# Kernel tuning notes

Hardware: AMD Instinct MI355X
Metric: run time of the kernel (lower is better)

The kernel has to match this reference:

```python
import jax, jax.numpy as jnp
import numpy as np

NUM_MODELS = 64
IN_F, HID, OUT_F = 6, 64, 3
LAYERS = 5
LN_EPS = 1e-5


def _mm_linear(x, W, B, idx):
    # W: [M, out, in], B: [M, out], x: [N, in], idx: [N]
    return jnp.einsum('nof,nf->no', W[idx], x) + B[idx]


def _mm_layernorm(x, g, b, idx):
    mu = jnp.mean(x, axis=-1, keepdims=True)
    var = jnp.mean((x - mu) ** 2, axis=-1, keepdims=True)
    xn = (x - mu) * jax.lax.rsqrt(var + LN_EPS)
    return xn * g[idx] + b[idx]


def setup_inputs() -> dict:
    key = jax.random.key(0)
    ks = jax.random.split(key, 16)
    N = 262144
    sqrt_k = float(np.sqrt(1.0 / NUM_MODELS))
    u = lambda k, shape: jax.random.uniform(k, shape, jnp.float32, -sqrt_k, sqrt_k)
    inp = {
        'x': jax.random.normal(ks[0], (N, IN_F), jnp.float32),
        'indices': jax.random.randint(ks[1], (N,), 0, NUM_MODELS),
        'W0': u(ks[2], (NUM_MODELS, HID, IN_F)), 'B0': u(ks[3], (NUM_MODELS, HID)),
        'G0': jnp.ones((NUM_MODELS, HID), jnp.float32), 'H0': jnp.zeros((NUM_MODELS, HID), jnp.float32),
        'W1': u(ks[4], (NUM_MODELS, HID, HID)), 'B1': u(ks[5], (NUM_MODELS, HID)),
        'G1': jnp.ones((NUM_MODELS, HID), jnp.float32), 'H1': jnp.zeros((NUM_MODELS, HID), jnp.float32),
        'W2': u(ks[6], (NUM_MODELS, HID, HID)), 'B2': u(ks[7], (NUM_MODELS, HID)),
        'G2': jnp.ones((NUM_MODELS, HID), jnp.float32), 'H2': jnp.zeros((NUM_MODELS, HID), jnp.float32),
        'W3': u(ks[8], (NUM_MODELS, HID, HID)), 'B3': u(ks[9], (NUM_MODELS, HID)),
        'G3': jnp.ones((NUM_MODELS, HID), jnp.float32), 'H3': jnp.zeros((NUM_MODELS, HID), jnp.float32),
        'W4': u(ks[10], (NUM_MODELS, OUT_F, HID)), 'B4': u(ks[11], (NUM_MODELS, OUT_F)),
    }
    return inp


def reference(x, indices, W0, B0, G0, H0, W1, B1, G1, H1, W2, B2, G2, H2, W3, B3, G3, H3, W4, B4):
    # forward_through_layers with use_layernorm=True, layers=5:
    Ws = [(W0, B0, G0, H0), (W1, B1, G1, H1), (W2, B2, G2, H2), (W3, B3, G3, H3)]
    h = x
    for W, B, G, Hb in Ws:
        h = _mm_linear(h, W, B, indices)
        h = _mm_layernorm(h, G, Hb, indices)
        h = jax.nn.relu(h)
    return _mm_linear(h, W4, B4, indices)  # [N, 3]
```

## Files before the change

kernel.cpp:

```cpp
#include <hip/hip_runtime.h>


#define NM    64
#define HIDD  64
#define INF   6
#define OUTF  3
#define CAP   4864
#define NBLK  256

#define O_COUNTS 0
#define O_HIST   64
#define O_BASE   (O_HIST + NBLK * 64)
#define O_ORDER  (O_BASE + NBLK * 64)
#define IWS_INTS (O_ORDER + NM * CAP)

#define CONST_B   30720
#define NCONSTF   784
#define IMG_BYTES 33856

#define HST 72

typedef _Float16 v8h __attribute__((ext_vector_type(8)));
typedef _Float16 v4h __attribute__((ext_vector_type(4)));
typedef float    v4f __attribute__((ext_vector_type(4)));

__global__ __launch_bounds__(256, 4) void hist_img_kernel(
    const int* __restrict__ idx, int n,
    const float* __restrict__ W0, const float* __restrict__ W1,
    const float* __restrict__ W2, const float* __restrict__ W3,
    const float* __restrict__ W4,
    const float* __restrict__ B0, const float* __restrict__ G0, const float* __restrict__ H0,
    const float* __restrict__ B1, const float* __restrict__ G1, const float* __restrict__ H1,
    const float* __restrict__ B2, const float* __restrict__ G2, const float* __restrict__ H2,
    const float* __restrict__ B3, const float* __restrict__ G3, const float* __restrict__ H3,
    const float* __restrict__ B4,
    int* __restrict__ iws, unsigned char* __restrict__ imgbase) {
    __shared__ int lc[NM];
    const int b = blockIdx.x, t = threadIdx.x;
    const int m = b >> 2, sub = b & 3;

    _Float16* img = (_Float16*)(imgbase + (size_t)m * IMG_BYTES);
    float* cst = (float*)(imgbase + (size_t)m * IMG_BYTES + CONST_B);
    for (int s = sub * 256 + t; s < 1920; s += 1024) {
        int f = s >> 6, l = s & 63;
        int c = l & 15, q = l >> 4;
        float vals[8];
        if (f < 4) {
            const float* wr = W0 + m * 384 + (f * 16 + c) * 6;
#pragma unroll
            for (int j = 0; j < 8; j++) {
                int k = q * 8 + j;
                vals[j] = (k < INF) ? wr[k] : 0.0f;
            }
        } else if (f < 28) {
            int ll = (f - 4) >> 3, fb = (f - 4) & 7;
            int mt = fb >> 1, kh = fb & 1;
            const float* W = (ll == 0) ? W1 : (ll == 1) ? W2 : W3;
            const float* wr = W + m * 4096 + (mt * 16 + c) * 64 + kh * 32 + q * 8;
#pragma unroll
            for (int j = 0; j < 8; j++) vals[j] = wr[j];
        } else {
            int kh = f - 28;
            const float* wr = W4 + m * 192 + c * 64 + kh * 32 + q * 8;
#pragma unroll
            for (int j = 0; j < 8; j++) vals[j] = (c < OUTF) ? wr[j] : 0.0f;
        }
        v8h o;
#pragma unroll
        for (int j = 0; j < 8; j++) o[j] = (_Float16)vals[j];
        *(v8h*)(img + (size_t)s * 8) = o;
    }
    {
        const float* lsrc[12] = {B0, G0, H0, B1, G1, H1, B2, G2, H2, B3, G3, H3};
        int e = sub * 256 + t;
        if (e < NCONSTF) {
            float v = 0.0f;
            if (e < 768) {
                int l = e / 192, r = e - l * 192;
                v = lsrc[l * 3 + (r >> 6)][m * 64 + (r & 63)];
            } else if (e < 771) {
                v = B4[m * 3 + (e - 768)];
            }
            cst[e] = v;
        }
    }

    if (t < NM) lc[t] = 0;
    __syncthreads();
    const int per = (n + NBLK - 1) / NBLK;
    const int beg = b * per, end = min(n, beg + per);
    for (int i = beg + t; i < end; i += 256) atomicAdd(&lc[idx[i]], 1);
    __syncthreads();
    if (t < NM) iws[O_HIST + b * NM + t] = lc[t];
}

__global__ void scan_kernel(int* __restrict__ iws) {
    const int m = threadIdx.x;
    int run = 0;
    for (int b = 0; b < NBLK; b++) {
        int v = iws[O_HIST + b * NM + m];
        iws[O_BASE + b * NM + m] = run;
        run += v;
    }
    iws[O_COUNTS + m] = run;
}

__global__ __launch_bounds__(256, 4) void scatter_kernel(
    const int* __restrict__ idx, const float* __restrict__ x, int n,
    int* __restrict__ iws, _Float16* __restrict__ xs) {
    __shared__ int lcnt[NM], lbase[NM];
    const int b = blockIdx.x, t = threadIdx.x;
    if (t < NM) lcnt[t] = 0;
    __syncthreads();
    const int per = (n + NBLK - 1) / NBLK;
    const int beg = b * per, end = min(n, beg + per);
    int sidq[4], mmq[4], rrq[4];
    int qn = 0;
    for (int i = beg + t; i < end; i += 256) {
        sidq[qn] = i;
        mmq[qn] = idx[i];
        rrq[qn] = atomicAdd(&lcnt[mmq[qn]], 1);
        qn++;
    }
    __syncthreads();
    if (t < NM) lbase[t] = iws[O_BASE + b * NM + t];
    __syncthreads();
    for (int j = 0; j < qn; j++) {
        int slot = mmq[j] * CAP + lbase[mmq[j]] + rrq[j];
        iws[O_ORDER + slot] = sidq[j];
        const float* xp = x + (size_t)sidq[j] * 6;
        float2 a0 = *(const float2*)(xp);
        float2 a1 = *(const float2*)(xp + 2);
        float2 a2 = *(const float2*)(xp + 4);
        v8h o = {};
        o[0] = (_Float16)a0.x; o[1] = (_Float16)a0.y;
        o[2] = (_Float16)a1.x; o[3] = (_Float16)a1.y;
        o[4] = (_Float16)a2.x; o[5] = (_Float16)a2.y;
        *(v8h*)(xs + (size_t)slot * 8) = o;
    }
}

__device__ __forceinline__ void layer_epilogue(v4f D[4], const v4f gg[4], const v4f hh[4],
                                               _Float16* __restrict__ st) {
    float S = 0.0f, Q2 = 0.0f;
#pragma unroll
    for (int mt = 0; mt < 4; mt++)
#pragma unroll
        for (int r = 0; r < 4; r++) {
            float v = D[mt][r];
            S += v;
            Q2 = fmaf(v, v, Q2);
        }
    S += __shfl_xor(S, 16, 64);
    S += __shfl_xor(S, 32, 64);
    Q2 += __shfl_xor(Q2, 16, 64);
    Q2 += __shfl_xor(Q2, 32, 64);
    float mu = S * (1.0f / 64.0f);
    float var = Q2 * (1.0f / 64.0f) - mu * mu;
    float rs = rsqrtf(var + 1e-5f);
#pragma unroll
    for (int mt = 0; mt < 4; mt++) {
        v4h o;
#pragma unroll
        for (int r = 0; r < 4; r++) {
            float a = gg[mt][r] * rs;
            float bb = fmaf(-mu, a, hh[mt][r]);
            o[r] = (_Float16)fmaxf(fmaf(D[mt][r], a, bb), 0.0f);
        }
        *(v4h*)(st + mt * 16) = o;
    }
}

__global__ __launch_bounds__(256, 4) void mlp_kernel(
    const int* __restrict__ iws, const _Float16* __restrict__ xs,
    const unsigned char* __restrict__ imgbase, float* __restrict__ out) {
    __shared__ __align__(16) _Float16 s_H[4 * 64 * HST];

    const int m = blockIdx.y;
    const int cnt = iws[O_COUNTS + m];
    const int beg = m * CAP, end = beg + cnt;
    const int base = beg + blockIdx.x * 256;
    if (base >= end) return;

    const int t = threadIdx.x, w = t >> 6, lane = t & 63;
    const int c = lane & 15, q = lane >> 4;
    const int wbase = base + w * 64;
    if (wbase >= end) return;

    const _Float16* img = (const _Float16*)(imgbase + (size_t)m * IMG_BYTES);
    const float* cf = (const float*)(imgbase + (size_t)m * IMG_BYTES + CONST_B);
    _Float16* Hw = s_H + w * (64 * HST);
    const int* order = iws + O_ORDER;

    int sid[4], sp[4];
#pragma unroll
    for (int ti = 0; ti < 4; ti++) {
        int p = wbase + ti * 16 + c;
        sp[ti] = p < end ? p : end - 1;
        sid[ti] = order[sp[ti]];
    }

    {
        v8h A[4];
#pragma unroll
        for (int mt = 0; mt < 4; mt++)
            A[mt] = *(const v8h*)(img + mt * 512 + lane * 8);
        v4f bias[4], gg[4], hh[4];
#pragma unroll
        for (int mt = 0; mt < 4; mt++) {
            bias[mt] = *(const v4f*)(cf + mt * 16 + q * 4);
            gg[mt]   = *(const v4f*)(cf + 64 + mt * 16 + q * 4);
            hh[mt]   = *(const v4f*)(cf + 128 + mt * 16 + q * 4);
        }
#pragma unroll
        for (int ti = 0; ti < 4; ti++) {
            v8h bfr = {};
            if (q == 0) bfr = *(const v8h*)(xs + (size_t)sp[ti] * 8);
            v4f D[4];
#pragma unroll
            for (int mt = 0; mt < 4; mt++)
                D[mt] = __builtin_amdgcn_mfma_f32_16x16x32_f16(A[mt], bfr, bias[mt], 0, 0, 0);
            layer_epilogue(D, gg, hh, Hw + (ti * 16 + c) * HST + q * 4);
        }
    }

#pragma unroll 1
    for (int l = 1; l <= 3; l++) {
        const _Float16* wp = img + 2048 + (l - 1) * 4096 + lane * 8;
        v8h A[4][2];
#pragma unroll
        for (int mt = 0; mt < 4; mt++)
#pragma unroll
            for (int kh = 0; kh < 2; kh++)
                A[mt][kh] = *(const v8h*)(wp + (mt * 2 + kh) * 512);
        const float* cb = cf + l * 192;
        v4f bias[4], gg[4], hh[4];
#pragma unroll
        for (int mt = 0; mt < 4; mt++) {
            bias[mt] = *(const v4f*)(cb + mt * 16 + q * 4);
            gg[mt]   = *(const v4f*)(cb + 64 + mt * 16 + q * 4);
            hh[mt]   = *(const v4f*)(cb + 128 + mt * 16 + q * 4);
        }
#pragma unroll
        for (int ti = 0; ti < 4; ti++) {
            const _Float16* hp = Hw + (ti * 16 + c) * HST;
            v8h b0 = *(const v8h*)(hp + q * 8);
            v8h b1 = *(const v8h*)(hp + 32 + q * 8);
            v4f D[4];
#pragma unroll
            for (int mt = 0; mt < 4; mt++) {
                D[mt] = __builtin_amdgcn_mfma_f32_16x16x32_f16(A[mt][0], b0, bias[mt], 0, 0, 0);
                D[mt] = __builtin_amdgcn_mfma_f32_16x16x32_f16(A[mt][1], b1, D[mt], 0, 0, 0);
            }
            layer_epilogue(D, gg, hh, Hw + (ti * 16 + c) * HST + q * 4);
        }
    }

    {
        const _Float16* wp = img + 14336 + lane * 8;
        v8h A0 = *(const v8h*)(wp);
        v8h A1 = *(const v8h*)(wp + 512);
        v4f b4i = {cf[768], cf[769], cf[770], 0.0f};
#pragma unroll
        for (int ti = 0; ti < 4; ti++) {
            const _Float16* hp = Hw + (ti * 16 + c) * HST;
            v8h b0 = *(const v8h*)(hp + q * 8);
            v8h b1 = *(const v8h*)(hp + 32 + q * 8);
            v4f D = __builtin_amdgcn_mfma_f32_16x16x32_f16(A0, b0, b4i, 0, 0, 0);
            D = __builtin_amdgcn_mfma_f32_16x16x32_f16(A1, b1, D, 0, 0, 0);
            int p = wbase + ti * 16 + c;
            if (q == 0 && p < end) {
                float* op = out + (size_t)sid[ti] * 3;
                op[0] = D[0]; op[1] = D[1]; op[2] = D[2];
            }
        }
    }
}

extern "C" void kernel_launch(void* const* d_in, const int* in_sizes, int n_in,
                              void* d_out, int out_size, void* d_ws, size_t ws_size,
                              hipStream_t stream) {
    const float* x  = (const float*)d_in[0];
    const int*  idx = (const int*)d_in[1];
    const float* W0 = (const float*)d_in[2];
    const float* B0 = (const float*)d_in[3];
    const float* G0 = (const float*)d_in[4];
    const float* H0 = (const float*)d_in[5];
    const float* W1 = (const float*)d_in[6];
    const float* B1 = (const float*)d_in[7];
    const float* G1 = (const float*)d_in[8];
    const float* H1 = (const float*)d_in[9];
    const float* W2 = (const float*)d_in[10];
    const float* B2 = (const float*)d_in[11];
    const float* G2 = (const float*)d_in[12];
    const float* H2 = (const float*)d_in[13];
    const float* W3 = (const float*)d_in[14];
    const float* B3 = (const float*)d_in[15];
    const float* G3 = (const float*)d_in[16];
    const float* H3 = (const float*)d_in[17];
    const float* W4 = (const float*)d_in[18];
    const float* B4 = (const float*)d_in[19];
    float* out = (float*)d_out;

    int n = in_sizes[1];
    int* iws = (int*)d_ws;
    _Float16* xs = (_Float16*)((char*)d_ws + (size_t)IWS_INTS * 4);
    unsigned char* imgbase =
        (unsigned char*)d_ws + (size_t)IWS_INTS * 4 + (size_t)NM * CAP * 16;

    hist_img_kernel<<<dim3(NBLK), 256, 0, stream>>>(
        idx, n, W0, W1, W2, W3, W4,
        B0, G0, H0, B1, G1, H1, B2, G2, H2, B3, G3, H3, B4, iws, imgbase);
    scan_kernel<<<1, 64, 0, stream>>>(iws);
    scatter_kernel<<<dim3(NBLK), 256, 0, stream>>>(idx, x, n, iws, xs);
    mlp_kernel<<<dim3(19, NM), 256, 0, stream>>>(iws, xs, imgbase, out);
}
```

Baseline: 146.9 us.

## Merge histogram, scan and scatter into one kernel using global atomic cursors

Replaces the three-kernel histogram/scan/scatter bucketing with one kernel. Each block counts its local histogram, reserves a range per model through a global atomicAdd on padded cursors (zeroed by a memset), then scatters rows directly. This removes two kernel launches and the serial scan, at the cost of nondeterministic row order inside each bucket. The grid drops to 128 blocks, and the layer loop in the MLP kernel is now fully unrolled.

```diff
diff --git a/kernel.cpp b/kernel.cpp
--- a/kernel.cpp
+++ b/kernel.cpp
@@ -6,13 +6,12 @@
 #define INF   6
 #define OUTF  3
 #define CAP   4864
-#define NBLK  256
-
-#define O_COUNTS 0
-#define O_HIST   64
-#define O_BASE   (O_HIST + NBLK * 64)
-#define O_ORDER  (O_BASE + NBLK * 64)
-#define IWS_INTS (O_ORDER + NM * CAP)
+#define NBLKB 128
+
+#define CSTRIDE   32
+#define O_CURSORS 0
+#define O_ORDER   2048
+#define IWS_INTS  (O_ORDER + NM * CAP)
 
 #define CONST_B   30720
 #define NCONSTF   784
@@ -24,8 +23,8 @@
 typedef _Float16 v4h __attribute__((ext_vector_type(4)));
 typedef float    v4f __attribute__((ext_vector_type(4)));
 
-__global__ __launch_bounds__(256, 4) void hist_img_kernel(
-    const int* __restrict__ idx, int n,
+__global__ __launch_bounds__(256, 4) void bucket_img_kernel(
+    const int* __restrict__ idx, const float* __restrict__ x, int n,
     const float* __restrict__ W0, const float* __restrict__ W1,
     const float* __restrict__ W2, const float* __restrict__ W3,
     const float* __restrict__ W4,
@@ -34,14 +33,15 @@
     const float* __restrict__ B2, const float* __restrict__ G2, const float* __restrict__ H2,
     const float* __restrict__ B3, const float* __restrict__ G3, const float* __restrict__ H3,
     const float* __restrict__ B4,
-    int* __restrict__ iws, unsigned char* __restrict__ imgbase) {
-    __shared__ int lc[NM];
+    int* __restrict__ iws, _Float16* __restrict__ xs,
+    unsigned char* __restrict__ imgbase) {
+    __shared__ int lcnt[NM], lcur[NM];
     const int b = blockIdx.x, t = threadIdx.x;
-    const int m = b >> 2, sub = b & 3;
+    const int m = b >> 1, sub = b & 1;
 
     _Float16* img = (_Float16*)(imgbase + (size_t)m * IMG_BYTES);
     float* cst = (float*)(imgbase + (size_t)m * IMG_BYTES + CONST_B);
-    for (int s = sub * 256 + t; s < 1920; s += 1024) {
+    for (int s = sub * 256 + t; s < 1920; s += 512) {
         int f = s >> 6, l = s & 63;
         int c = l & 15, q = l >> 4;
         float vals[8];
@@ -70,65 +70,32 @@
         for (int j = 0; j < 8; j++) o[j] = (_Float16)vals[j];
         *(v8h*)(img + (size_t)s * 8) = o;
     }
-    {
+    for (int e = sub * 256 + t; e < NCONSTF; e += 512) {
         const float* lsrc[12] = {B0, G0, H0, B1, G1, H1, B2, G2, H2, B3, G3, H3};
-        int e = sub * 256 + t;
-        if (e < NCONSTF) {
-            float v = 0.0f;
-            if (e < 768) {
-                int l = e / 192, r = e - l * 192;
-                v = lsrc[l * 3 + (r >> 6)][m * 64 + (r & 63)];
-            } else if (e < 771) {
-                v = B4[m * 3 + (e - 768)];
-            }
-            cst[e] = v;
-        }
-    }
-
-    if (t < NM) lc[t] = 0;
-    __syncthreads();
-    const int per = (n + NBLK - 1) / NBLK;
-    const int beg = b * per, end = min(n, beg + per);
-    for (int i = beg + t; i < end; i += 256) atomicAdd(&lc[idx[i]], 1);
-    __syncthreads();
-    if (t < NM) iws[O_HIST + b * NM + t] = lc[t];
-}
-
-__global__ void scan_kernel(int* __restrict__ iws) {
-    const int m = threadIdx.x;
-    int run = 0;
-    for (int b = 0; b < NBLK; b++) {
-        int v = iws[O_HIST + b * NM + m];
-        iws[O_BASE + b * NM + m] = run;
-        run += v;
-    }
-    iws[O_COUNTS + m] = run;
-}
-
-__global__ __launch_bounds__(256, 4) void scatter_kernel(
-    const int* __restrict__ idx, const float* __restrict__ x, int n,
-    int* __restrict__ iws, _Float16* __restrict__ xs) {
-    __shared__ int lcnt[NM], lbase[NM];
-    const int b = blockIdx.x, t = threadIdx.x;
+        float v = 0.0f;
+        if (e < 768) {
+            int l = e / 192, r = e - l * 192;
+            v = lsrc[l * 3 + (r >> 6)][m * 64 + (r & 63)];
+        } else if (e < 771) {
+            v = B4[m * 3 + (e - 768)];
+        }
+        cst[e] = v;
+    }
+
     if (t < NM) lcnt[t] = 0;
     __syncthreads();
-    const int per = (n + NBLK - 1) / NBLK;
+    const int per = (n + NBLKB - 1) / NBLKB;
     const int beg = b * per, end = min(n, beg + per);
-    int sidq[4], mmq[4], rrq[4];
-    int qn = 0;
+    for (int i = beg + t; i < end; i += 256) atomicAdd(&lcnt[idx[i]], 1);
+    __syncthreads();
+    if (t < NM) lcur[t] = atomicAdd(&iws[O_CURSORS + t * CSTRIDE], lcnt[t]);
+    __syncthreads();
     for (int i = beg + t; i < end; i += 256) {
-        sidq[qn] = i;
-        mmq[qn] = idx[i];
-        rrq[qn] = atomicAdd(&lcnt[mmq[qn]], 1);
-        qn++;
-    }
-    __syncthreads();
-    if (t < NM) lbase[t] = iws[O_BASE + b * NM + t];
-    __syncthreads();
-    for (int j = 0; j < qn; j++) {
-        int slot = mmq[j] * CAP + lbase[mmq[j]] + rrq[j];
-        iws[O_ORDER + slot] = sidq[j];
-        const float* xp = x + (size_t)sidq[j] * 6;
+        int mm = idx[i];
+        int r = atomicAdd(&lcur[mm], 1);
+        int slot = mm * CAP + r;
+        iws[O_ORDER + slot] = i;
+        const float* xp = x + (size_t)i * 6;
         float2 a0 = *(const float2*)(xp);
         float2 a1 = *(const float2*)(xp + 2);
         float2 a2 = *(const float2*)(xp + 4);
@@ -177,7 +144,7 @@
     __shared__ __align__(16) _Float16 s_H[4 * 64 * HST];
 
     const int m = blockIdx.y;
-    const int cnt = iws[O_COUNTS + m];
+    const int cnt = iws[O_CURSORS + m * CSTRIDE];
     const int beg = m * CAP, end = beg + cnt;
     const int base = beg + blockIdx.x * 256;
     if (base >= end) return;
@@ -224,7 +191,7 @@
         }
     }
 
-#pragma unroll 1
+#pragma unroll
     for (int l = 1; l <= 3; l++) {
         const _Float16* wp = img + 2048 + (l - 1) * 4096 + lane * 8;
         v8h A[4][2];
@@ -308,10 +275,9 @@
     unsigned char* imgbase =
         (unsigned char*)d_ws + (size_t)IWS_INTS * 4 + (size_t)NM * CAP * 16;
 
-    hist_img_kernel<<<dim3(NBLK), 256, 0, stream>>>(
-        idx, n, W0, W1, W2, W3, W4,
-        B0, G0, H0, B1, G1, H1, B2, G2, H2, B3, G3, H3, B4, iws, imgbase);
-    scan_kernel<<<1, 64, 0, stream>>>(iws);
-    scatter_kernel<<<dim3(NBLK), 256, 0, stream>>>(idx, x, n, iws, xs);
+    hipMemsetAsync(d_ws, 0, NM * CSTRIDE * sizeof(int), stream);
+    bucket_img_kernel<<<dim3(NBLKB), 256, 0, stream>>>(
+        idx, x, n, W0, W1, W2, W3, W4,
+        B0, G0, H0, B1, G1, H1, B2, G2, H2, B3, G3, H3, B4, iws, xs, imgbase);
     mlp_kernel<<<dim3(19, NM), 256, 0, stream>>>(iws, xs, imgbase, out);
 }
```

New measurement: 136.5 us. 7.0% less time.
